# Kernel optimization log

Measured on AMD Instinct MI355X. Metric: run time of the kernel, lower is better.

## Reference

```python
import jax, jax.numpy as jnp
import numpy as np
from jax import lax

H, W = 32, 32
HEADS = 8
EPS_LN = 1e-5


def layer_norm(x, g, b):
    mu = jnp.mean(x, axis=-1, keepdims=True)
    var = jnp.mean((x - mu) ** 2, axis=-1, keepdims=True)
    return (x - mu) * lax.rsqrt(var + EPS_LN) * g + b


def l2norm(x):  # F.normalize along last dim, eps=1e-12
    n = jnp.sqrt(jnp.sum(x * x, axis=-1, keepdims=True))
    return x / jnp.maximum(n, 1e-12)


def channel_attention(x, qkv_w, temp, proj_w, proj_b):
    B, N, C = x.shape
    d = C // HEADS
    qkv = (x @ qkv_w).reshape(B, N, 3, HEADS, d).transpose(2, 0, 3, 1, 4)  # [3,B,h,N,d]
    q, k, v = qkv[0], qkv[1], qkv[2]
    q = l2norm(q.swapaxes(-2, -1))  # [B,h,d,N], normalized over N
    k = l2norm(k.swapaxes(-2, -1))
    v = v.swapaxes(-2, -1)          # [B,h,d,N]
    attn = jnp.einsum('bhdn,bhen->bhde', q, k) * temp  # [B,h,d,d]
    attn = jax.nn.softmax(attn, axis=-1)
    out = jnp.einsum('bhde,bhen->bhdn', attn, v)       # [B,h,d,N]
    out = out.transpose(0, 3, 1, 2).reshape(B, N, C)
    return out @ proj_w + proj_b


def cross_attention(x1, x2, rp_w, rp_b, cn_g, cn_b):
    # head_count = 1 (efficient/linear attention)
    B, N, D = x1.shape
    keys = x2.swapaxes(1, 2)            # [B,D,N]
    values = x1.swapaxes(1, 2)          # [B,D,N]
    key = jax.nn.softmax(keys, axis=2)  # softmax over tokens
    query = jax.nn.softmax(keys, axis=1)  # softmax over channels
    context = jnp.einsum('bdn,ben->bde', key, values)     # [B,Dk,Dv]
    attended = jnp.einsum('bde,bdn->ben', context, query)  # [B,Dv,N]
    agg = attended.reshape(B, D, H, W)
    # 1x1 conv reprojection D -> 2D
    rep = jnp.einsum('bdhw,ed->behw', agg, rp_w) + rp_b[None, :, None, None]
    rep = rep.reshape(B, 2 * D, N).transpose(0, 2, 1)     # [B,N,2D]
    return layer_norm(rep, cn_g, cn_b)


def mix_ffn(x, fc1_w, fc1_b, dw_w, dw_b, fc2_w, fc2_b):
    B, N, _ = x.shape
    c2 = fc1_w.shape[1]
    h1 = x @ fc1_w + fc1_b                                 # [B,N,c2]
    t = h1.swapaxes(1, 2).reshape(B, c2, H, W)
    conv = lax.conv_general_dilated(
        t, dw_w, window_strides=(1, 1), padding='SAME',
        feature_group_count=c2,
        dimension_numbers=('NCHW', 'OIHW', 'NCHW')) + dw_b[None, :, None, None]
    h2 = conv.reshape(B, c2, N).swapaxes(1, 2)             # [B,N,c2]
    return jax.nn.gelu(h2, approximate=False) @ fc2_w + fc2_b


def reference(x1, x2, ln1_g, ln1_b, ca_qkv_w, ca_temp, ca_proj_w, ca_proj_b,
              ln3_g, ln3_b, rp_w, rp_b, cn_g, cn_b, ln2_g, ln2_b,
              fc1_w, fc1_b, dw_w, dw_b, fc2_w, fc2_b):
    # NOTE: original code uses norm1 + channel_attn1 on BOTH streams
    channel1 = x1 + channel_attention(layer_norm(x1, ln1_g, ln1_b), ca_qkv_w, ca_temp, ca_proj_w, ca_proj_b)
    channel2 = x2 + channel_attention(layer_norm(x2, ln1_g, ln1_b), ca_qkv_w, ca_temp, ca_proj_w, ca_proj_b)
    n1 = layer_norm(channel1, ln3_g, ln3_b)
    n2 = layer_norm(channel2, ln3_g, ln3_b)
    attn = cross_attention(n1, n2, rp_w, rp_b, cn_g, cn_b)
    tx = jnp.concatenate([channel1, channel2], axis=2) + attn  # [B,N,2D]
    mx = tx + mix_ffn(layer_norm(tx, ln2_g, ln2_b), fc1_w, fc1_b, dw_w, dw_b, fc2_w, fc2_b)
    return mx


def setup_inputs() -> dict:
    key = jax.random.key(0)
    ks = jax.random.split(key, 8)
    B, N, D = 16, 1024, 384
    s = 0.02
    return {
        'x1': jax.random.normal(ks[0], (B, N, D), jnp.float32),
        'x2': jax.random.normal(ks[1], (B, N, D), jnp.float32),
        'ln1_g': jnp.ones((D,), jnp.float32), 'ln1_b': jnp.zeros((D,), jnp.float32),
        'ca_qkv_w': jax.random.normal(ks[2], (D, 3 * D), jnp.float32) * s,
        'ca_temp': jnp.ones((HEADS, 1, 1), jnp.float32),
        'ca_proj_w': jax.random.normal(ks[3], (D, D), jnp.float32) * s,
        'ca_proj_b': jnp.zeros((D,), jnp.float32),
        'ln3_g': jnp.ones((D,), jnp.float32), 'ln3_b': jnp.zeros((D,), jnp.float32),
        'rp_w': jax.random.normal(ks[4], (2 * D, D), jnp.float32) * s,
        'rp_b': jnp.zeros((2 * D,), jnp.float32),
        'cn_g': jnp.ones((2 * D,), jnp.float32), 'cn_b': jnp.zeros((2 * D,), jnp.float32),
        'ln2_g': jnp.ones((2 * D,), jnp.float32), 'ln2_b': jnp.zeros((2 * D,), jnp.float32),
        'fc1_w': jax.random.normal(ks[5], (2 * D, 4 * D), jnp.float32) * s,
        'fc1_b': jnp.zeros((4 * D,), jnp.float32),
        'dw_w': jax.random.normal(ks[6], (4 * D, 1, 3, 3), jnp.float32) * s,
        'dw_b': jnp.zeros((4 * D,), jnp.float32),
        'fc2_w': jax.random.normal(ks[7], (4 * D, 2 * D), jnp.float32) * s,
        'fc2_b': jnp.zeros((2 * D,), jnp.float32),
    }
```

## Files before the change

### kernel.cpp

```cpp
#include <hip/hip_runtime.h>
#include <math.h>

#define BN 16
#define NN 1024
#define DD 384
#define D2 768
#define C2 1536
#define NHEAD 8
#define DH 48

#define SZ_ND   (BN*NN*DD)
#define SZ_N2D  (BN*NN*D2)
#define SZ_NC2  (BN*NN*C2)

typedef __bf16 bf16x8 __attribute__((ext_vector_type(8)));
typedef float f32x4v __attribute__((ext_vector_type(4)));
typedef unsigned short u16x4 __attribute__((ext_vector_type(4)));

__device__ __forceinline__ unsigned short f2bf(float x){
  unsigned int u = __float_as_uint(x);
  u += 0x7FFFu + ((u >> 16) & 1u);
  return (unsigned short)(u >> 16);
}
__device__ __forceinline__ float bf2f(unsigned short h){
  return __uint_as_float(((unsigned int)h) << 16);
}

__device__ __forceinline__ float blockReduceSum256(float v){
  __shared__ float red[4];
  #pragma unroll
  for (int o=32;o;o>>=1) v += __shfl_down(v,o,64);
  if ((threadIdx.x&63)==0) red[threadIdx.x>>6]=v;
  __syncthreads();
  float r = red[0]+red[1]+red[2]+red[3];
  __syncthreads();
  return r;
}
__device__ __forceinline__ float blockReduceMax256(float v){
  __shared__ float red[4];
  #pragma unroll
  for (int o=32;o;o>>=1) v = fmaxf(v, __shfl_down(v,o,64));
  if ((threadIdx.x&63)==0) red[threadIdx.x>>6]=v;
  __syncthreads();
  float r = fmaxf(fmaxf(red[0],red[1]),fmaxf(red[2],red[3]));
  __syncthreads();
  return r;
// ... 28 lines not shown
  float v=0.f;
  for (int i=threadIdx.x;i<C;i+=256){ float d = x[i]-mu; v += d*d; }
  v = blockReduceSum256(v);
  const float rs = rsqrtf(v/(float)C + 1e-5f);
  unsigned short* ohp = oh + (size_t)row*C;
  unsigned short* olp = ol + (size_t)row*C;
  for (int i=threadIdx.x;i<C;i+=256){
    float val = (x[i]-mu)*rs*g[i] + b[i];
    unsigned short hh = f2bf(val);
    ohp[i] = hh; olp[i] = f2bf(val - bf2f(hh));
  }
}

__global__ __launch_bounds__(256) void rowsoftmax_split_kernel(const float* __restrict__ in,
    unsigned short* __restrict__ oh, unsigned short* __restrict__ ol, int C){
  const int row = blockIdx.x;
  const float* x = in + (size_t)row*C;
  float m = -3.0e38f;
  for (int i=threadIdx.x;i<C;i+=256) m = fmaxf(m, x[i]);
  m = blockReduceMax256(m);
  float s = 0.f;
  for (int i=threadIdx.x;i<C;i+=256) s += expf(x[i]-m);
  s = blockReduceSum256(s);
  const float inv = 1.f/s;
  unsigned short* ohp = oh + (size_t)row*C;
  unsigned short* olp = ol + (size_t)row*C;
  for (int i=threadIdx.x;i<C;i+=256){
    float p = expf(x[i]-m)*inv;
    unsigned short hh = f2bf(p);
    ohp[i] = hh; olp[i] = f2bf(p - bf2f(hh));
  }
}

__global__ __launch_bounds__(256) void colsoftmax_kernel(const float* __restrict__ in,
    float* __restrict__ out){
  const int dl = threadIdx.x & 63;
  const int nc = threadIdx.x >> 6;
  const int d  = blockIdx.x*64 + dl;
  const int b  = blockIdx.y;
  const float* p = in + (size_t)b*NN*DD + d;
  __shared__ float redm[4][64];
  __shared__ float reds[4][64];
  float m = -3.0e38f;
  for (int n=nc*256; n<nc*256+256; n++) m = fmaxf(m, p[(size_t)n*DD]);
  redm[nc][dl] = m; __syncthreads();
  m = fmaxf(fmaxf(redm[0][dl],redm[1][dl]),fmaxf(redm[2][dl],redm[3][dl]));
  float s=0.f;
  for (int n=nc*256;n<nc*256+256;n++) s += expf(p[(size_t)n*DD]-m);
  reds[nc][dl]=s; __syncthreads();
  s = reds[0][dl]+reds[1][dl]+reds[2][dl]+reds[3][dl];
  const float inv = 1.f/s;
  float* q = out + (size_t)b*NN*DD + d;
  for (int n=nc*256;n<nc*256+256;n++) q[(size_t)n*DD] = expf(p[(size_t)n*DD]-m)*inv;
}

__global__ __launch_bounds__(256) void tsplit_kernel(const float* __restrict__ in,
    unsigned short* __restrict__ oh, unsigned short* __restrict__ ol, int R, int Cc){
  const size_t zb = (size_t)blockIdx.z * R * Cc;
  const float* ip = in + zb;
  unsigned short* ohp = oh + zb;
  unsigned short* olp = ol + zb;
  __shared__ float tile[32][33];
  const int c0 = blockIdx.x*32, r0 = blockIdx.y*32;
  const int j = threadIdx.x & 31, i4 = threadIdx.x >> 5;
  #pragma unroll
  for (int s=0;s<4;s++){
    int i = i4*4+s;
    tile[i][j] = ip[(size_t)(r0+i)*Cc + c0 + j];
  }
  __syncthreads();
  #pragma unroll
  for (int s=0;s<4;s++){
    int i = i4*4+s;
    float x = tile[j][i];
    unsigned short h = f2bf(x);
    ohp[(size_t)(c0+i)*R + r0 + j] = h;
    olp[(size_t)(c0+i)*R + r0 + j] = f2bf(x - bf2f(h));
  }
}

__global__ __launch_bounds__(256) void chattn_mfma_kernel(
    const float* __restrict__ qkv, const float* __restrict__ temp,
    unsigned short* __restrict__ coh, unsigned short* __restrict__ col)
{
  const int bh = blockIdx.x, b = bh >> 3, h = bh & 7;
  const int t = threadIdx.x, w = t >> 6, lane = t & 63;
  const int lr = lane & 15, g = lane >> 4;

  __shared__ __align__(16) unsigned char ldsA[27648];
  unsigned short (*Qh)[72] = (unsigned short(*)[72])(ldsA);
  unsigned short (*Ql)[72] = (unsigned short(*)[72])(ldsA + 6912);
  unsigned short (*Kh)[72] = (unsigned short(*)[72])(ldsA + 13824);
  unsigned short (*Kl)[72] = (unsigned short(*)[72])(ldsA + 20736);
  unsigned short (*Vh)[72] = (unsigned short(*)[72])(ldsA);
  unsigned short (*Vl)[72] = (unsigned short(*)[72])(ldsA + 9216);
  __shared__ unsigned short Ph[48][72], Pl[48][72];
  __shared__ float S[48][49];
  __shared__ float qn[48], kn[48];

  const size_t base = (size_t)b*NN*1152 + (size_t)h*48;

  int agrp[3], apr[3], aoff[3];
  #pragma unroll
  for (int l=0;l<3;l++){
    int idx = l*256+t;
    int mo = (idx>=384) ? 1 : 0;
    int a = idx - mo*384;
    agrp[l] = a%12; apr[l] = a/12; aoff[l] = mo*384;
  }

  f32x4v acc[12];
  #pragma unroll
  for (int i=0;i<12;i++) acc[i] = (f32x4v){0.f,0.f,0.f,0.f};

  float4 cur[3][2];
  #pragma unroll
  for (int l=0;l<3;l++){
    const float* p = qkv + base + (size_t)(apr[l]*2)*1152 + aoff[l] + agrp[l]*4;
    cur[l][0] = *(const float4*)p;
    cur[l][1] = *(const float4*)(p+1152);
  }

  for (int nc=0; nc<16; nc++){
    #pragma unroll
    for (int l=0;l<3;l++){
      unsigned short (*Dh)[72] = aoff[l] ? Kh : Qh;
      unsigned short (*Dl)[72] = aoff[l] ? Kl : Ql;
      const float x0[4] = {cur[l][0].x, cur[l][0].y, cur[l][0].z, cur[l][0].w};
      const float x1[4] = {cur[l][1].x, cur[l][1].y, cur[l][1].z, cur[l][1].w};
      #pragma unroll
      for (int c=0;c<4;c++){
        int d = agrp[l]*4+c;
        unsigned short h0 = f2bf(x0[c]), h1 = f2bf(x1[c]);
        unsigned short l0 = f2bf(x0[c]-bf2f(h0)), l1 = f2bf(x1[c]-bf2f(h1));
        *(unsigned int*)&Dh[d][apr[l]*2] = (unsigned)h0 | ((unsigned)h1<<16);
        *(unsigned int*)&Dl[d][apr[l]*2] = (unsigned)l0 | ((unsigned)l1<<16);
      }
    }
    __syncthreads();
    if (nc < 15){
      #pragma unroll
      for (int l=0;l<3;l++){
        const float* p = qkv + base + (size_t)((nc+1)*64 + apr[l]*2)*1152 + aoff[l] + agrp[l]*4;
        cur[l][0] = *(const float4*)p;
        cur[l][1] = *(const float4*)(p+1152);
      }
    }
    if (w < 3){
      #pragma unroll
      for (int ks=0;ks<2;ks++){
        bf16x8 a_h = *(const bf16x8*)&Qh[w*16+lr][ks*32+g*8];
        bf16x8 a_l = *(const bf16x8*)&Ql[w*16+lr][ks*32+g*8];
        #pragma unroll
        for (int c=0;c<3;c++){
          bf16x8 b_h = *(const bf16x8*)&Kh[c*16+lr][ks*32+g*8];
          bf16x8 b_l = *(const bf16x8*)&Kl[c*16+lr][ks*32+g*8];
          acc[c] = __builtin_amdgcn_mfma_f32_16x16x32_bf16(a_h, b_h, acc[c], 0,0,0);
          acc[c] = __builtin_amdgcn_mfma_f32_16x16x32_bf16(a_l, b_h, acc[c], 0,0,0);
          acc[c] = __builtin_amdgcn_mfma_f32_16x16x32_bf16(a_h, b_l, acc[c], 0,0,0);
        }
      }
    } else {
      #pragma unroll
      for (int ks=0;ks<2;ks++){
        #pragma unroll
        for (int c=0;c<3;c++){
          bf16x8 qh_ = *(const bf16x8*)&Qh[c*16+lr][ks*32+g*8];
          bf16x8 ql_ = *(const bf16x8*)&Ql[c*16+lr][ks*32+g*8];
          bf16x8 kh_ = *(const bf16x8*)&Kh[c*16+lr][ks*32+g*8];
          bf16x8 kl_ = *(const bf16x8*)&Kl[c*16+lr][ks*32+g*8];
          acc[c]   = __builtin_amdgcn_mfma_f32_16x16x32_bf16(qh_, qh_, acc[c],   0,0,0);
          acc[3+c] = __builtin_amdgcn_mfma_f32_16x16x32_bf16(qh_, ql_, acc[3+c], 0,0,0);
          acc[6+c] = __builtin_amdgcn_mfma_f32_16x16x32_bf16(kh_, kh_, acc[6+c], 0,0,0);
          acc[9+c] = __builtin_amdgcn_mfma_f32_16x16x32_bf16(kh_, kl_, acc[9+c], 0,0,0);
        }
      }
    }
    __syncthreads();
  }

  const float tp = temp[h];
  if (w == 3){
    if ((lane>>4) == ((lane&15)>>2)){
      int p = lane & 15, r = p & 3;
      #pragma unroll
      for (int c=0;c<3;c++){
        float q2 = fmaxf(acc[c][r]   + 2.f*acc[3+c][r], 0.f);
        float k2 = fmaxf(acc[6+c][r] + 2.f*acc[9+c][r], 0.f);
        qn[c*16+p] = fmaxf(sqrtf(q2), 1e-12f);
        kn[c*16+p] = fmaxf(sqrtf(k2), 1e-12f);
      }
    }
  }
  __syncthreads();
  if (w < 3){
    #pragma unroll
    for (int c=0;c<3;c++){
      #pragma unroll
      for (int r=0;r<4;r++){
        int i = w*16 + g*4 + r, j = c*16 + lr;
        S[i][j] = acc[c][r]*tp/(qn[i]*kn[j]);
      }
    }
  }
  __syncthreads();

  int vgrp[3], vtk[3];
  #pragma unroll
  for (int l=0;l<3;l++){ int idx=l*256+t; vtk[l]=idx/12; vgrp[l]=idx%12; }
  float4 pv[3];
  #pragma unroll
  for (int l=0;l<3;l++)
    pv[l] = *(const float4*)(qkv + base + (size_t)vtk[l]*1152 + 768 + vgrp[l]*4);

  if (t < 48){
    float m = -3.0e38f;
    for (int j=0;j<48;j++) m = fmaxf(m, S[t][j]);
    float s = 0.f;
    for (int j=0;j<48;j++){ float e_ = expf(S[t][j]-m); S[t][j] = e_; s += e_; }
    float inv = 1.f/s;
    for (int j=0;j<48;j++){
      float p = S[t][j]*inv;
      unsigned short hp = f2bf(p);
      Ph[t][j] = hp; Pl[t][j] = f2bf(p - bf2f(hp));
    }
    #pragma unroll
    for (int j=48;j<64;j++){ Ph[t][j]=0; Pl[t][j]=0; }
  } else {
    const u16x4 z4 = (u16x4){0,0,0,0};
    for (int idx=t-48; idx<512; idx+=208){
      int tk = idx>>3, q = idx&7;
      if (q<4) *(u16x4*)&Vh[tk][48+(q&3)*4] = z4;
      else     *(u16x4*)&Vl[tk][48+(q&3)*4] = z4;
    }
  }
  __syncthreads();

  bf16x8 pfh[3][2], pfl[3][2];
  #pragma unroll
  for (int it=0;it<3;it++)
    #pragma unroll
    for (int ks=0;ks<2;ks++){
      pfh[it][ks] = *(const bf16x8*)&Ph[it*16+lr][ks*32+g*8];
      pfl[it][ks] = *(const bf16x8*)&Pl[it*16+lr][ks*32+g*8];
    }

  for (int vc=0; vc<16; vc++){
    #pragma unroll
    for (int l=0;l<3;l++){
      const float xv[4] = {pv[l].x, pv[l].y, pv[l].z, pv[l].w};
      u16x4 hv, lv;
      #pragma unroll
      for (int c=0;c<4;c++){
        unsigned short hh = f2bf(xv[c]);
        hv[c] = hh; lv[c] = f2bf(xv[c] - bf2f(hh));
      }
      *(u16x4*)&Vh[vtk[l]][vgrp[l]*4] = hv;
      *(u16x4*)&Vl[vtk[l]][vgrp[l]*4] = lv;
    }
    __syncthreads();
    if (vc < 15){
      #pragma unroll
      for (int l=0;l<3;l++)
        pv[l] = *(const float4*)(qkv + base + (size_t)((vc+1)*64+vtk[l])*1152 + 768 + vgrp[l]*4);
    }
    bf16x8 vfh[2], vfl[2];
    #pragma unroll
    for (int ks=0;ks<2;ks++){
      vfh[ks] = *(const bf16x8*)&Vh[w*16+lr][ks*32+g*8];
      vfl[ks] = *(const bf16x8*)&Vl[w*16+lr][ks*32+g*8];
    }
    f32x4v o[3];
    #pragma unroll
    for (int it=0;it<3;it++) o[it] = (f32x4v){0.f,0.f,0.f,0.f};
    #pragma unroll
    for (int it=0;it<3;it++)
      #pragma unroll
      for (int ks=0;ks<2;ks++){
        o[it] = __builtin_amdgcn_mfma_f32_16x16x32_bf16(pfh[it][ks], vfh[ks], o[it], 0,0,0);
        o[it] = __builtin_amdgcn_mfma_f32_16x16x32_bf16(pfl[it][ks], vfh[ks], o[it], 0,0,0);
        o[it] = __builtin_amdgcn_mfma_f32_16x16x32_bf16(pfh[it][ks], vfl[ks], o[it], 0,0,0);
      }
    const int n = vc*64 + w*16 + lr;
    #pragma unroll
    for (int it=0;it<3;it++){
      const size_t off = ((size_t)b*NN + n)*DD + h*48 + it*16 + g*4;
      u16x4 hv, lv;
      #pragma unroll
      for (int r=0;r<4;r++){
        float x = o[it][r];
        unsigned short hh = f2bf(x);
        hv[r] = hh; lv[r] = f2bf(x - bf2f(hh));
      }
      *(u16x4*)(coh + off) = hv;
      *(u16x4*)(col + off) = lv;
    }
    __syncthreads();
  }
}

__global__ __launch_bounds__(256) void wconv_t_kernel(const float* __restrict__ in,
    unsigned short* __restrict__ oh, unsigned short* __restrict__ ol, int K, int N){
  __shared__ float tile[32][33];
  const int n0 = blockIdx.x*32, k0 = blockIdx.y*32;
  const int j = threadIdx.x & 31, i4 = threadIdx.x >> 5;
  #pragma unroll
  for (int s=0;s<4;s++){
    int i = i4*4+s;
    tile[i][j] = in[(size_t)(k0+i)*N + n0 + j];
  }
  __syncthreads();
  #pragma unroll
  for (int s=0;s<4;s++){
    int i = i4*4+s;
    float x = tile[j][i];
    unsigned short h = f2bf(x);
    oh[(size_t)(n0+i)*K + k0 + j] = h;
    ol[(size_t)(n0+i)*K + k0 + j] = f2bf(x - bf2f(h));
  }
}

__global__ __launch_bounds__(256) void wconv_kernel(const float* __restrict__ in,
    unsigned short* __restrict__ oh, unsigned short* __restrict__ ol, int n){
  int i = blockIdx.x*256 + threadIdx.x;
  if (i < n){
    float x = in[i];
    unsigned short h = f2bf(x);
    oh[i] = h;
    ol[i] = f2bf(x - bf2f(h));
  }
}

template<bool BIAS_, bool RES_, bool SPLIT_>
__global__ __launch_bounds__(256) void gemm_bf16x3s_kernel(
    const unsigned short* __restrict__ Ah, const unsigned short* __restrict__ Al,
    const unsigned short* __restrict__ Bh, const unsigned short* __restrict__ Bl,
    const float* __restrict__ bias, const float* __restrict__ res,
    float* __restrict__ C, unsigned short* __restrict__ Ch, unsigned short* __restrict__ Cl,
    int M, int N, int K, size_t sAz, size_t sBz, size_t sCz)
{
  const int t = threadIdx.x;
  const int nwg = gridDim.x*gridDim.y;
// ... 99 lines not shown
      for (int mi=0;mi<4;mi++){
        const int r0 = m0 + wm*64 + mi*16 + g*4;
        #pragma unroll
        for (int r=0;r<4;r++){
          float v = acc[mi][ni][r];
          unsigned short hv = f2bf(v);
          const size_t off = (size_t)(r0+r)*N + col;
          Chb[off] = hv;
          Clb[off] = f2bf(v - bf2f(hv));
        }
      }
    }
  } else {
    float* Cb = C + zo*sCz;
    const float* resb = RES_ ? (res + zo*sCz) : nullptr;
    #pragma unroll
    for (int ni=0;ni<4;ni++){
      const int col = n0 + wn*64 + ni*16 + lr;
      const float bb = BIAS_ ? bias[col] : 0.f;
      #pragma unroll
      for (int mi=0;mi<4;mi++){
        const int r0 = m0 + wm*64 + mi*16 + g*4;
        #pragma unroll
        for (int r=0;r<4;r++){
          float v = acc[mi][ni][r] + bb;
          if (RES_) v += resb[(size_t)(r0+r)*N + col];
          Cb[(size_t)(r0+r)*N + col] = v;
        }
      }
    }
  }
}

__global__ __launch_bounds__(256) void ln_concat_kernel(const float* __restrict__ rep,
    const float* __restrict__ g, const float* __restrict__ b,
    const float* __restrict__ ch1, const float* __restrict__ ch2,
    float* __restrict__ tx){
  const int row = blockIdx.x;
  const float* x = rep + (size_t)row*D2;
  float s=0.f;
  for (int i=threadIdx.x;i<D2;i+=256) s += x[i];
  s = blockReduceSum256(s);
  const float mu = s / (float)D2;
  float v=0.f;
  for (int i=threadIdx.x;i<D2;i+=256){ float d = x[i]-mu; v += d*d; }
  v = blockReduceSum256(v);
  const float rs = rsqrtf(v/(float)D2 + 1e-5f);
  float* o = tx + (size_t)row*D2;
  for (int i=threadIdx.x;i<D2;i+=256){
    float val = (x[i]-mu)*rs*g[i] + b[i];
    float rv = (i<DD) ? ch1[(size_t)row*DD + i] : ch2[(size_t)row*DD + i - DD];
    o[i] = val + rv;
  }
}

__global__ __launch_bounds__(256) void dwconv_gelu_kernel(const float* __restrict__ h1,
    const float* __restrict__ w, const float* __restrict__ bias,
    unsigned short* __restrict__ gh, unsigned short* __restrict__ gl){
  const int idx = blockIdx.x*256 + threadIdx.x;
  const int b   = idx / 12288;
  const int r   = idx - b*12288;
  const int hh  = r / 384;
  const int c4  = r - hh*384;
  const int c   = c4*4;
  const float* base = h1 + (size_t)b*NN*C2 + c;
  const size_t obase = ((size_t)b*NN + hh*32)*C2 + c;

  f32x4v wk[9];
  #pragma unroll
  for (int k=0;k<9;k++){
    f32x4v t_;
    #pragma unroll
    for (int q=0;q<4;q++) t_[q] = w[(size_t)(c+q)*9 + k];
    wk[k] = t_;
  }
  f32x4v bvv;
  {
    const float4 bb = *(const float4*)(bias + c);
    bvv = (f32x4v){bb.x, bb.y, bb.z, bb.w};
  }

  const bool hm = (hh > 0), hp = (hh < 31);
  const f32x4v z4 = (f32x4v){0.f,0.f,0.f,0.f};
  const size_t rm = (size_t)((hh-1)*32)*C2;
  const size_t r0 = (size_t)( hh   *32)*C2;
// ... 40 lines not shown

extern "C" void kernel_launch(void* const* d_in, const int* in_sizes, int n_in,
                              void* d_out, int out_size, void* d_ws, size_t ws_size,
                              hipStream_t stream) {
  const float* x1     = (const float*)d_in[0];
  const float* x2     = (const float*)d_in[1];
  const float* ln1_g  = (const float*)d_in[2];
  const float* ln1_b  = (const float*)d_in[3];
  const float* qkv_w  = (const float*)d_in[4];
  const float* ca_temp= (const float*)d_in[5];
  const float* proj_w = (const float*)d_in[6];
  const float* proj_b = (const float*)d_in[7];
  const float* ln3_g  = (const float*)d_in[8];
  const float* ln3_b  = (const float*)d_in[9];
  const float* rp_w   = (const float*)d_in[10];
  const float* rp_b   = (const float*)d_in[11];
  const float* cn_g   = (const float*)d_in[12];
  const float* cn_b   = (const float*)d_in[13];
  const float* ln2_g  = (const float*)d_in[14];
  const float* ln2_b  = (const float*)d_in[15];
  const float* fc1_w  = (const float*)d_in[16];
  const float* fc1_b  = (const float*)d_in[17];
  const float* dw_w   = (const float*)d_in[18];
  const float* dw_b   = (const float*)d_in[19];
  const float* fc2_w  = (const float*)d_in[20];
  const float* fc2_b  = (const float*)d_in[21];
  float* out = (float*)d_out;
  float* W   = (float*)d_ws;

  unsigned short* ycoh = (unsigned short*)W;
  unsigned short* ycol = ycoh + (size_t)SZ_ND;
  unsigned short* coh  = ycoh;
  unsigned short* col  = ycol;
  float* qkvb = W + (size_t)SZ_ND;
  float* ch1  = W + 25165824ull;
  float* ch2  = W + 31457280ull;
  unsigned short* qkvwT_h  = (unsigned short*)(W + 37748736ull);
  unsigned short* qkvwT_l  = qkvwT_h + 442368u;
  unsigned short* projwT_h = qkvwT_l + 442368u;
  unsigned short* projwT_l = projwT_h + 147456u;
  float* n1  = W;
  float* n2  = W + (size_t)SZ_ND;
  float* KS  = W + 2ull*SZ_ND;
  unsigned short* QSh = (unsigned short*)(W + 3ull*SZ_ND);
  unsigned short* QSl = QSh + (size_t)SZ_ND;
  unsigned short* rpw_h = (unsigned short*)(W + 37748736ull);
  unsigned short* rpw_l = rpw_h + 294912u;
  unsigned short* n1t_h = (unsigned short*)(W + 38043648ull);
  unsigned short* n1t_l = n1t_h + (size_t)SZ_ND;
  unsigned short* KSt_h = (unsigned short*)(W + (size_t)SZ_ND);
  unsigned short* KSt_l = KSt_h + (size_t)SZ_ND;
  unsigned short* ctxT_h = (unsigned short*)W;
  unsigned short* ctxT_l = ctxT_h + 2359296u;
  unsigned short* ATbh = (unsigned short*)(W + 2ull*SZ_ND);
  unsigned short* ATbl = ATbh + (size_t)SZ_ND;
  float* rep = W;
  float* txp  = out;
  float* h1   = W;
  unsigned short* y2h = (unsigned short*)(W + 25165824ull);
  unsigned short* y2l = y2h + (size_t)SZ_N2D;
  unsigned short* fc1wT_h = (unsigned short*)(W + 37748736ull);
  unsigned short* fc1wT_l = fc1wT_h + 1179648u;
  unsigned short* gh = (unsigned short*)(W + 25165824ull);
  unsigned short* gl = gh + (size_t)SZ_NC2;
  unsigned short* fc2wT_h = (unsigned short*)W;
  unsigned short* fc2wT_l = fc2wT_h + 1179648u;

  const int M = BN*NN;

  wconv_t_kernel<<<dim3(1152/32, DD/32), dim3(256), 0, stream>>>(qkv_w, qkvwT_h, qkvwT_l, DD, 1152);
  wconv_t_kernel<<<dim3(DD/32, DD/32), dim3(256), 0, stream>>>(proj_w, projwT_h, projwT_l, DD, DD);

  ln_split_kernel<<<dim3(M), dim3(256), 0, stream>>>(x1, ln1_g, ln1_b, ycoh, ycol, DD);
  gemm_bf16x3s_kernel<false,false,false><<<dim3(1152/128, M/128), dim3(256), 0, stream>>>(
      ycoh, ycol, qkvwT_h, qkvwT_l, nullptr, nullptr, qkvb, nullptr, nullptr, M, 1152, DD, 0,0,0);
  chattn_mfma_kernel<<<dim3(BN*NHEAD), dim3(256), 0, stream>>>(qkvb, ca_temp, coh, col);
  gemm_bf16x3s_kernel<true,true,false><<<dim3(DD/128, M/128), dim3(256), 0, stream>>>(
      coh, col, projwT_h, projwT_l, proj_b, x1, ch1, nullptr, nullptr, M, DD, DD, 0,0,0);

  ln_split_kernel<<<dim3(M), dim3(256), 0, stream>>>(x2, ln1_g, ln1_b, ycoh, ycol, DD);
  gemm_bf16x3s_kernel<false,false,false><<<dim3(1152/128, M/128), dim3(256), 0, stream>>>(
      ycoh, ycol, qkvwT_h, qkvwT_l, nullptr, nullptr, qkvb, nullptr, nullptr, M, 1152, DD, 0,0,0);
  chattn_mfma_kernel<<<dim3(BN*NHEAD), dim3(256), 0, stream>>>(qkvb, ca_temp, coh, col);
  gemm_bf16x3s_kernel<true,true,false><<<dim3(DD/128, M/128), dim3(256), 0, stream>>>(
      coh, col, projwT_h, projwT_l, proj_b, x2, ch2, nullptr, nullptr, M, DD, DD, 0,0,0);

  wconv_kernel<<<dim3(294912/256), dim3(256), 0, stream>>>(rp_w, rpw_h, rpw_l, 294912);
  ln_kernel<<<dim3(M), dim3(256), 0, stream>>>(ch1, ln3_g, ln3_b, n1, DD);
  ln_kernel<<<dim3(M), dim3(256), 0, stream>>>(ch2, ln3_g, ln3_b, n2, DD);
  rowsoftmax_split_kernel<<<dim3(M), dim3(256), 0, stream>>>(n2, QSh, QSl, DD);
  colsoftmax_kernel<<<dim3(DD/64, BN), dim3(256), 0, stream>>>(n2, KS);
  tsplit_kernel<<<dim3(DD/32, NN/32, BN), dim3(256), 0, stream>>>(n1, n1t_h, n1t_l, NN, DD);
  tsplit_kernel<<<dim3(DD/32, NN/32, BN), dim3(256), 0, stream>>>(KS, KSt_h, KSt_l, NN, DD);
  gemm_bf16x3s_kernel<false,false,true><<<dim3(DD/128, DD/128, BN), dim3(256), 0, stream>>>(
      n1t_h, n1t_l, KSt_h, KSt_l, nullptr, nullptr, nullptr, ctxT_h, ctxT_l,
      DD, DD, NN, (size_t)DD*NN, (size_t)DD*NN, (size_t)DD*DD);
  gemm_bf16x3s_kernel<false,false,true><<<dim3(DD/128, NN/128, BN), dim3(256), 0, stream>>>(
      QSh, QSl, ctxT_h, ctxT_l, nullptr, nullptr, nullptr, ATbh, ATbl,
      NN, DD, DD, (size_t)NN*DD, (size_t)DD*DD, (size_t)NN*DD);
  gemm_bf16x3s_kernel<true,false,false><<<dim3(D2/128, M/128), dim3(256), 0, stream>>>(
      ATbh, ATbl, rpw_h, rpw_l, rp_b, nullptr, rep, nullptr, nullptr, M, D2, DD, 0,0,0);
  ln_concat_kernel<<<dim3(M), dim3(256), 0, stream>>>(rep, cn_g, cn_b, ch1, ch2, txp);

  wconv_t_kernel<<<dim3(C2/32, D2/32), dim3(256), 0, stream>>>(fc1_w, fc1wT_h, fc1wT_l, D2, C2);
  ln_split_kernel<<<dim3(M), dim3(256), 0, stream>>>(txp, ln2_g, ln2_b, y2h, y2l, D2);
  gemm_bf16x3s_kernel<true,false,false><<<dim3(C2/128, M/128), dim3(256), 0, stream>>>(
      y2h, y2l, fc1wT_h, fc1wT_l, fc1_b, nullptr, h1, nullptr, nullptr, M, C2, D2, 0,0,0);
  dwconv_gelu_kernel<<<dim3(196608/256), dim3(256), 0, stream>>>(h1, dw_w, dw_b, gh, gl);
  wconv_t_kernel<<<dim3(D2/32, C2/32), dim3(256), 0, stream>>>(fc2_w, fc2wT_h, fc2wT_l, C2, D2);
  gemm_bf16x3s_kernel<true,true,false><<<dim3(D2/128, M/128), dim3(256), 0, stream>>>(
      gh, gl, fc2wT_h, fc2wT_l, fc2_b, txp, out, nullptr, nullptr, M, D2, C2, 0,0,0);
}
```

Before: 965.5 us.

## Add 256x256 double-buffered bf16x3 GEMM and fuse LN2 into concat

Adds a 256x256-tile, 512-thread bf16x3 split-precision GEMM with double-buffered XOR-swizzled LDS and workgroup swizzling. It is used for the QKV, reprojection, fc1 and fc2 GEMMs, and the QKV weight is zero-padded to 1280 columns so the grid tiles evenly. Larger tiles aim to raise operand reuse and MFMA density. Separately, the concat LayerNorm now also computes LN2 and writes the split bf16 outputs directly, removing one full pass over the activation. The trade-offs are heavy register and LDS use per block and fewer blocks on the smaller GEMMs (D2=768 gives only 3 column tiles).

```diff
diff --git a/kernel.cpp b/kernel.cpp
--- a/kernel.cpp
+++ b/kernel.cpp
@@ -374,14 +374,14 @@
 }
 
 __global__ __launch_bounds__(256) void wconv_t_kernel(const float* __restrict__ in,
-    unsigned short* __restrict__ oh, unsigned short* __restrict__ ol, int K, int N){
+    unsigned short* __restrict__ oh, unsigned short* __restrict__ ol, int K, int Nin){
   __shared__ float tile[32][33];
   const int n0 = blockIdx.x*32, k0 = blockIdx.y*32;
   const int j = threadIdx.x & 31, i4 = threadIdx.x >> 5;
   #pragma unroll
   for (int s=0;s<4;s++){
     int i = i4*4+s;
-    tile[i][j] = in[(size_t)(k0+i)*N + n0 + j];
+    tile[i][j] = (n0 + j < Nin) ? in[(size_t)(k0+i)*Nin + n0 + j] : 0.f;
   }
   __syncthreads();
   #pragma unroll
@@ -547,25 +547,167 @@
   }
 }
 
-__global__ __launch_bounds__(256) void ln_concat_kernel(const float* __restrict__ rep,
-    const float* __restrict__ g, const float* __restrict__ b,
+template<bool BIAS_, bool RES_>
+__global__ __launch_bounds__(512, 2) void gemm_bf16x3_256_kernel(
+    const unsigned short* __restrict__ Ah, const unsigned short* __restrict__ Al,
+    const unsigned short* __restrict__ Bh, const unsigned short* __restrict__ Bl,
+    const float* __restrict__ bias, const float* __restrict__ res,
+    float* __restrict__ C, int M, int Ncr, int K)
+{
+  const int t = threadIdx.x;
+  const int nwg = gridDim.x*gridDim.y;
+  const int lin = blockIdx.y*gridDim.x + blockIdx.x;
+  const int swz = ((nwg & 7)==0) ? ((lin & 7)*(nwg >> 3) + (lin >> 3)) : lin;
+  const int bx = swz % gridDim.x, by = swz / gridDim.x;
+  const int m0 = by*256, n0 = bx*256;
+
+  __shared__ unsigned short As_h0[256][32], As_l0[256][32];
+  __shared__ unsigned short Bs_h0[256][32], Bs_l0[256][32];
+  __shared__ unsigned short As_h1[256][32], As_l1[256][32];
+  __shared__ unsigned short Bs_h1[256][32], Bs_l1[256][32];
+
+  const unsigned short* Ahb = Ah + (size_t)m0*K;
+  const unsigned short* Alb = Al + (size_t)m0*K;
+  const unsigned short* Bhb = Bh + (size_t)n0*K;
+  const unsigned short* Blb = Bl + (size_t)n0*K;
+
+  f32x4v acc[8][4];
+  #pragma unroll
+  for (int i=0;i<8;i++)
+    #pragma unroll
+    for (int j=0;j<4;j++) acc[i][j] = (f32x4v){0.f,0.f,0.f,0.f};
+
+  const int w  = t >> 6;
+  const int wm = w >> 2, wn = w & 3;
+  const int lr = t & 15, g = (t & 63) >> 4;
+  const int srow = t >> 1;
+  const int kb0  = (t & 1)*2;
+  const int ssw  = (srow >> 1) & 3;
+  const int ks0  = ((kb0+0) ^ ssw)*8;
+  const int ks1  = ((kb0+1) ^ ssw)*8;
+
+  uint4 rAh0,rAh1,rAl0,rAl1,rBh0,rBh1,rBl0,rBl1;
+
+#define LOADT(K0) { \
+    const size_t go0 = (size_t)srow*K + (size_t)(K0) + (size_t)(kb0*8); \
+    rAh0 = *(const uint4*)(Ahb + go0); rAh1 = *(const uint4*)(Ahb + go0 + 8); \
+    rAl0 = *(const uint4*)(Alb + go0); rAl1 = *(const uint4*)(Alb + go0 + 8); \
+    rBh0 = *(const uint4*)(Bhb + go0); rBh1 = *(const uint4*)(Bhb + go0 + 8); \
+    rBl0 = *(const uint4*)(Blb + go0); rBl1 = *(const uint4*)(Blb + go0 + 8); }
+
+#define WRITET(BUF) { \
+    *(uint4*)&As_h##BUF[srow][ks0] = rAh0; *(uint4*)&As_h##BUF[srow][ks1] = rAh1; \
+    *(uint4*)&As_l##BUF[srow][ks0] = rAl0; *(uint4*)&As_l##BUF[srow][ks1] = rAl1; \
+    *(uint4*)&Bs_h##BUF[srow][ks0] = rBh0; *(uint4*)&Bs_h##BUF[srow][ks1] = rBh1; \
+    *(uint4*)&Bs_l##BUF[srow][ks0] = rBl0; *(uint4*)&Bs_l##BUF[srow][ks1] = rBl1; }
+
+#define COMPUTET(BUF) { \
+    bf16x8 bhf[4], blf[4]; \
+    _Pragma("unroll") \
+    for (int ni=0;ni<4;ni++){ \
+      const int rb = wn*64 + ni*16 + lr; \
+      const int kb = (g ^ ((rb>>1)&3))*8; \
+      bhf[ni] = *(const bf16x8*)&Bs_h##BUF[rb][kb]; \
+      blf[ni] = *(const bf16x8*)&Bs_l##BUF[rb][kb]; \
+    } \
+    _Pragma("unroll") \
+    for (int mi=0;mi<8;mi++){ \
+      const int ra = wm*128 + mi*16 + lr; \
+      const int ka = (g ^ ((ra>>1)&3))*8; \
+      bf16x8 ah_ = *(const bf16x8*)&As_h##BUF[ra][ka]; \
+      bf16x8 al_ = *(const bf16x8*)&As_l##BUF[ra][ka]; \
+      _Pragma("unroll") \
+      for (int ni=0;ni<4;ni++){ \
+        f32x4v c_ = acc[mi][ni]; \
+        c_ = __builtin_amdgcn_mfma_f32_16x16x32_bf16(ah_, bhf[ni], c_, 0,0,0); \
+        c_ = __builtin_amdgcn_mfma_f32_16x16x32_bf16(al_, bhf[ni], c_, 0,0,0); \
+        c_ = __builtin_amdgcn_mfma_f32_16x16x32_bf16(ah_, blf[ni], c_, 0,0,0); \
+        acc[mi][ni] = c_; \
+      } \
+    } }
+
+  const int nk = K >> 5;
+  LOADT(0);
+  WRITET(0);
+  LOADT(32);
+  __syncthreads();
+
+  for (int kt = 0; kt < nk; kt += 2){
+    COMPUTET(0);
+    if (kt+1 < nk) WRITET(1);
+    if (kt+2 < nk) LOADT((kt+2)*32);
+    __syncthreads();
+    if (kt+1 < nk) COMPUTET(1);
+    if (kt+2 < nk) WRITET(0);
+    if (kt+3 < nk) LOADT((kt+3)*32);
+    __syncthreads();
+  }
+
+#undef LOADT
+#undef WRITET
+#undef COMPUTET
+
+  #pragma unroll
+  for (int ni=0;ni<4;ni++){
+    const int col = n0 + wn*64 + ni*16 + lr;
+    if (col < Ncr){
+      const float bb = BIAS_ ? bias[col] : 0.f;
+      #pragma unroll
+      for (int mi=0;mi<8;mi++){
+        const int r0 = m0 + wm*128 + mi*16 + g*4;
+        #pragma unroll
+        for (int r=0;r<4;r++){
+          float v = acc[mi][ni][r] + bb;
+          if (RES_) v += res[(size_t)(r0+r)*Ncr + col];
+          C[(size_t)(r0+r)*Ncr + col] = v;
+        }
+      }
+    }
+  }
+}
+
+__global__ __launch_bounds__(256) void ln_concat_ln2_kernel(const float* __restrict__ rep,
+    const float* __restrict__ g1, const float* __restrict__ b1,
     const float* __restrict__ ch1, const float* __restrict__ ch2,
-    float* __restrict__ tx){
+    const float* __restrict__ g2, const float* __restrict__ b2,
+    float* __restrict__ tx, unsigned short* __restrict__ y2h, unsigned short* __restrict__ y2l){
   const int row = blockIdx.x;
   const float* x = rep + (size_t)row*D2;
+  float xv[3];
   float s=0.f;
-  for (int i=threadIdx.x;i<D2;i+=256) s += x[i];
+  #pragma unroll
+  for (int q=0;q<3;q++){ xv[q] = x[threadIdx.x + q*256]; s += xv[q]; }
   s = blockReduceSum256(s);
   const float mu = s / (float)D2;
   float v=0.f;
-  for (int i=threadIdx.x;i<D2;i+=256){ float d = x[i]-mu; v += d*d; }
+  #pragma unroll
+  for (int q=0;q<3;q++){ float d = xv[q]-mu; v += d*d; }
   v = blockReduceSum256(v);
   const float rs = rsqrtf(v/(float)D2 + 1e-5f);
-  float* o = tx + (size_t)row*D2;
-  for (int i=threadIdx.x;i<D2;i+=256){
-    float val = (x[i]-mu)*rs*g[i] + b[i];
+  float tv[3];
+  #pragma unroll
+  for (int q=0;q<3;q++){
+    int i = threadIdx.x + q*256;
+    float val = (xv[q]-mu)*rs*g1[i] + b1[i];
     float rv = (i<DD) ? ch1[(size_t)row*DD + i] : ch2[(size_t)row*DD + i - DD];
-    o[i] = val + rv;
+    tv[q] = val + rv;
+    tx[(size_t)row*D2 + i] = tv[q];
+  }
+  float s2 = tv[0]+tv[1]+tv[2];
+  s2 = blockReduceSum256(s2);
+  const float mu2 = s2 / (float)D2;
+  float v2=0.f;
+  #pragma unroll
+  for (int q=0;q<3;q++){ float d = tv[q]-mu2; v2 += d*d; }
+  v2 = blockReduceSum256(v2);
+  const float rs2 = rsqrtf(v2/(float)D2 + 1e-5f);
+  #pragma unroll
+  for (int q=0;q<3;q++){
+    int i = threadIdx.x + q*256;
+    float y = (tv[q]-mu2)*rs2*g2[i] + b2[i];
+    unsigned short hh = f2bf(y);
+    y2h[(size_t)row*D2 + i] = hh;
+    y2l[(size_t)row*D2 + i] = f2bf(y - bf2f(hh));
   }
 }
 
@@ -676,8 +818,8 @@
   float* ch1  = W + 25165824ull;
   float* ch2  = W + 31457280ull;
   unsigned short* qkvwT_h  = (unsigned short*)(W + 37748736ull);
-  unsigned short* qkvwT_l  = qkvwT_h + 442368u;
-  unsigned short* projwT_h = qkvwT_l + 442368u;
+  unsigned short* qkvwT_l  = qkvwT_h + 491520u;
+  unsigned short* projwT_h = qkvwT_l + 491520u;
   unsigned short* projwT_l = projwT_h + 147456u;
   float* n1  = W;
   float* n2  = W + (size_t)SZ_ND;
@@ -708,19 +850,19 @@
 
   const int M = BN*NN;
 
-  wconv_t_kernel<<<dim3(1152/32, DD/32), dim3(256), 0, stream>>>(qkv_w, qkvwT_h, qkvwT_l, DD, 1152);
+  wconv_t_kernel<<<dim3(1280/32, DD/32), dim3(256), 0, stream>>>(qkv_w, qkvwT_h, qkvwT_l, DD, 1152);
   wconv_t_kernel<<<dim3(DD/32, DD/32), dim3(256), 0, stream>>>(proj_w, projwT_h, projwT_l, DD, DD);
 
   ln_split_kernel<<<dim3(M), dim3(256), 0, stream>>>(x1, ln1_g, ln1_b, ycoh, ycol, DD);
-  gemm_bf16x3s_kernel<false,false,false><<<dim3(1152/128, M/128), dim3(256), 0, stream>>>(
-      ycoh, ycol, qkvwT_h, qkvwT_l, nullptr, nullptr, qkvb, nullptr, nullptr, M, 1152, DD, 0,0,0);
+  gemm_bf16x3_256_kernel<false,false><<<dim3(1280/256, M/256), dim3(512), 0, stream>>>(
+      ycoh, ycol, qkvwT_h, qkvwT_l, nullptr, nullptr, qkvb, M, 1152, DD);
   chattn_mfma_kernel<<<dim3(BN*NHEAD), dim3(256), 0, stream>>>(qkvb, ca_temp, coh, col);
   gemm_bf16x3s_kernel<true,true,false><<<dim3(DD/128, M/128), dim3(256), 0, stream>>>(
       coh, col, projwT_h, projwT_l, proj_b, x1, ch1, nullptr, nullptr, M, DD, DD, 0,0,0);
 
   ln_split_kernel<<<dim3(M), dim3(256), 0, stream>>>(x2, ln1_g, ln1_b, ycoh, ycol, DD);
-  gemm_bf16x3s_kernel<false,false,false><<<dim3(1152/128, M/128), dim3(256), 0, stream>>>(
-      ycoh, ycol, qkvwT_h, qkvwT_l, nullptr, nullptr, qkvb, nullptr, nullptr, M, 1152, DD, 0,0,0);
+  gemm_bf16x3_256_kernel<false,false><<<dim3(1280/256, M/256), dim3(512), 0, stream>>>(
+      ycoh, ycol, qkvwT_h, qkvwT_l, nullptr, nullptr, qkvb, M, 1152, DD);
   chattn_mfma_kernel<<<dim3(BN*NHEAD), dim3(256), 0, stream>>>(qkvb, ca_temp, coh, col);
   gemm_bf16x3s_kernel<true,true,false><<<dim3(DD/128, M/128), dim3(256), 0, stream>>>(
       coh, col, projwT_h, projwT_l, proj_b, x2, ch2, nullptr, nullptr, M, DD, DD, 0,0,0);
@@ -738,16 +880,16 @@
   gemm_bf16x3s_kernel<false,false,true><<<dim3(DD/128, NN/128, BN), dim3(256), 0, stream>>>(
       QSh, QSl, ctxT_h, ctxT_l, nullptr, nullptr, nullptr, ATbh, ATbl,
       NN, DD, DD, (size_t)NN*DD, (size_t)DD*DD, (size_t)NN*DD);
-  gemm_bf16x3s_kernel<true,false,false><<<dim3(D2/128, M/128), dim3(256), 0, stream>>>(
-      ATbh, ATbl, rpw_h, rpw_l, rp_b, nullptr, rep, nullptr, nullptr, M, D2, DD, 0,0,0);
-  ln_concat_kernel<<<dim3(M), dim3(256), 0, stream>>>(rep, cn_g, cn_b, ch1, ch2, txp);
+  gemm_bf16x3_256_kernel<true,false><<<dim3(D2/256, M/256), dim3(512), 0, stream>>>(
+      ATbh, ATbl, rpw_h, rpw_l, rp_b, nullptr, rep, M, D2, DD);
+  ln_concat_ln2_kernel<<<dim3(M), dim3(256), 0, stream>>>(
+      rep, cn_g, cn_b, ch1, ch2, ln2_g, ln2_b, txp, y2h, y2l);
 
   wconv_t_kernel<<<dim3(C2/32, D2/32), dim3(256), 0, stream>>>(fc1_w, fc1wT_h, fc1wT_l, D2, C2);
-  ln_split_kernel<<<dim3(M), dim3(256), 0, stream>>>(txp, ln2_g, ln2_b, y2h, y2l, D2);
-  gemm_bf16x3s_kernel<true,false,false><<<dim3(C2/128, M/128), dim3(256), 0, stream>>>(
-      y2h, y2l, fc1wT_h, fc1wT_l, fc1_b, nullptr, h1, nullptr, nullptr, M, C2, D2, 0,0,0);
+  gemm_bf16x3_256_kernel<true,false><<<dim3(C2/256, M/256), dim3(512), 0, stream>>>(
+      y2h, y2l, fc1wT_h, fc1wT_l, fc1_b, nullptr, h1, M, C2, D2);
   dwconv_gelu_kernel<<<dim3(196608/256), dim3(256), 0, stream>>>(h1, dw_w, dw_b, gh, gl);
   wconv_t_kernel<<<dim3(D2/32, C2/32), dim3(256), 0, stream>>>(fc2_w, fc2wT_h, fc2wT_l, C2, D2);
-  gemm_bf16x3s_kernel<true,true,false><<<dim3(D2/128, M/128), dim3(256), 0, stream>>>(
-      gh, gl, fc2wT_h, fc2wT_l, fc2_b, txp, out, nullptr, nullptr, M, D2, C2, 0,0,0);
-}
+  gemm_bf16x3_256_kernel<true,true><<<dim3(D2/256, M/256), dim3(512), 0, stream>>>(
+      gh, gl, fc2wT_h, fc2wT_l, fc2_b, txp, out, M, D2, C2);
+}
```

After: 1.056 ms. 1.09x slower.

## Fuse split/transposes into producers: bf16 QKV output, colsoftmax-transpose, LN-concat-LN2

Applied to the files above, without the earlier changes.

The QKV GEMM now writes hi/lo bf16 split outputs directly, so the channel-attention kernel loads bf16 pairs instead of fp32 and skips its own split. Column softmax writes transposed hi/lo bf16 directly, which removes a separate tsplit pass. The concat layer norm is fused with the following LN2 split, which drops one kernel and its reread of txp. The aim is to cut memory traffic and launches, but the colsoftmax transposed store is strided per thread and may coalesce poorly. The workspace layout also changes, so buffers must not overlap.

```diff
diff --git a/kernel.cpp b/kernel.cpp
--- a/kernel.cpp
+++ b/kernel.cpp
@@ -12,6 +12,7 @@
 #define SZ_ND   (BN*NN*DD)
 #define SZ_N2D  (BN*NN*D2)
 #define SZ_NC2  (BN*NN*C2)
+#define SZ_QKV  (BN*NN*3*DD)
 
 typedef __bf16 bf16x8 __attribute__((ext_vector_type(8)));
 typedef float f32x4v __attribute__((ext_vector_type(4)));
@@ -106,8 +107,8 @@
   }
 }
 
-__global__ __launch_bounds__(256) void colsoftmax_kernel(const float* __restrict__ in,
-    float* __restrict__ out){
+__global__ __launch_bounds__(256) void colsoftmax_tsplit_kernel(const float* __restrict__ in,
+    unsigned short* __restrict__ oh, unsigned short* __restrict__ ol){
   const int dl = threadIdx.x & 63;
   const int nc = threadIdx.x >> 6;
   const int d  = blockIdx.x*64 + dl;
@@ -124,8 +125,13 @@
   reds[nc][dl]=s; __syncthreads();
   s = reds[0][dl]+reds[1][dl]+reds[2][dl]+reds[3][dl];
   const float inv = 1.f/s;
-  float* q = out + (size_t)b*NN*DD + d;
-  for (int n=nc*256;n<nc*256+256;n++) q[(size_t)n*DD] = expf(p[(size_t)n*DD]-m)*inv;
+  unsigned short* qh = oh + ((size_t)b*DD + d)*NN;
+  unsigned short* ql = ol + ((size_t)b*DD + d)*NN;
+  for (int n=nc*256;n<nc*256+256;n++){
+    float val = expf(p[(size_t)n*DD]-m)*inv;
+    unsigned short hh = f2bf(val);
+    qh[n] = hh; ql[n] = f2bf(val - bf2f(hh));
+  }
 }
 
 __global__ __launch_bounds__(256) void tsplit_kernel(const float* __restrict__ in,
@@ -154,7 +160,8 @@
 }
 
 __global__ __launch_bounds__(256) void chattn_mfma_kernel(
-    const float* __restrict__ qkv, const float* __restrict__ temp,
+    const unsigned short* __restrict__ qh, const unsigned short* __restrict__ ql,
+    const float* __restrict__ temp,
     unsigned short* __restrict__ coh, unsigned short* __restrict__ col)
 {
   const int bh = blockIdx.x, b = bh >> 3, h = bh & 7;
@@ -187,12 +194,14 @@
   #pragma unroll
   for (int i=0;i<12;i++) acc[i] = (f32x4v){0.f,0.f,0.f,0.f};
 
-  float4 cur[3][2];
+  u16x4 ch0[3], ch1_[3], cl0[3], cl1[3];
   #pragma unroll
   for (int l=0;l<3;l++){
-    const float* p = qkv + base + (size_t)(apr[l]*2)*1152 + aoff[l] + agrp[l]*4;
-    cur[l][0] = *(const float4*)p;
-    cur[l][1] = *(const float4*)(p+1152);
+    const size_t a = base + (size_t)(apr[l]*2)*1152 + aoff[l] + agrp[l]*4;
+    ch0[l] = *(const u16x4*)(qh + a);
+    ch1_[l]= *(const u16x4*)(qh + a + 1152);
+    cl0[l] = *(const u16x4*)(ql + a);
+    cl1[l] = *(const u16x4*)(ql + a + 1152);
   }
 
   for (int nc=0; nc<16; nc++){
@@ -200,24 +209,22 @@
     for (int l=0;l<3;l++){
       unsigned short (*Dh)[72] = aoff[l] ? Kh : Qh;
       unsigned short (*Dl)[72] = aoff[l] ? Kl : Ql;
-      const float x0[4] = {cur[l][0].x, cur[l][0].y, cur[l][0].z, cur[l][0].w};
-      const float x1[4] = {cur[l][1].x, cur[l][1].y, cur[l][1].z, cur[l][1].w};
       #pragma unroll
       for (int c=0;c<4;c++){
         int d = agrp[l]*4+c;
-        unsigned short h0 = f2bf(x0[c]), h1 = f2bf(x1[c]);
-        unsigned short l0 = f2bf(x0[c]-bf2f(h0)), l1 = f2bf(x1[c]-bf2f(h1));
-        *(unsigned int*)&Dh[d][apr[l]*2] = (unsigned)h0 | ((unsigned)h1<<16);
-        *(unsigned int*)&Dl[d][apr[l]*2] = (unsigned)l0 | ((unsigned)l1<<16);
+        *(unsigned int*)&Dh[d][apr[l]*2] = (unsigned)ch0[l][c] | ((unsigned)ch1_[l][c]<<16);
+        *(unsigned int*)&Dl[d][apr[l]*2] = (unsigned)cl0[l][c] | ((unsigned)cl1[l][c]<<16);
       }
     }
     __syncthreads();
     if (nc < 15){
       #pragma unroll
       for (int l=0;l<3;l++){
-        const float* p = qkv + base + (size_t)((nc+1)*64 + apr[l]*2)*1152 + aoff[l] + agrp[l]*4;
-        cur[l][0] = *(const float4*)p;
-        cur[l][1] = *(const float4*)(p+1152);
+        const size_t a = base + (size_t)((nc+1)*64 + apr[l]*2)*1152 + aoff[l] + agrp[l]*4;
+        ch0[l] = *(const u16x4*)(qh + a);
+        ch1_[l]= *(const u16x4*)(qh + a + 1152);
+        cl0[l] = *(const u16x4*)(ql + a);
+        cl1[l] = *(const u16x4*)(ql + a + 1152);
       }
     }
     if (w < 3){
@@ -282,10 +289,13 @@
   int vgrp[3], vtk[3];
   #pragma unroll
   for (int l=0;l<3;l++){ int idx=l*256+t; vtk[l]=idx/12; vgrp[l]=idx%12; }
-  float4 pv[3];
-  #pragma unroll
-  for (int l=0;l<3;l++)
-    pv[l] = *(const float4*)(qkv + base + (size_t)vtk[l]*1152 + 768 + vgrp[l]*4);
+  u16x4 pvh[3], pvl[3];
+  #pragma unroll
+  for (int l=0;l<3;l++){
+    const size_t a = base + (size_t)vtk[l]*1152 + 768 + vgrp[l]*4;
+    pvh[l] = *(const u16x4*)(qh + a);
+    pvl[l] = *(const u16x4*)(ql + a);
+  }
 
   if (t < 48){
     float m = -3.0e38f;
@@ -322,21 +332,17 @@
   for (int vc=0; vc<16; vc++){
     #pragma unroll
     for (int l=0;l<3;l++){
-      const float xv[4] = {pv[l].x, pv[l].y, pv[l].z, pv[l].w};
-      u16x4 hv, lv;
-      #pragma unroll
-      for (int c=0;c<4;c++){
-        unsigned short hh = f2bf(xv[c]);
-        hv[c] = hh; lv[c] = f2bf(xv[c] - bf2f(hh));
-      }
-      *(u16x4*)&Vh[vtk[l]][vgrp[l]*4] = hv;
-      *(u16x4*)&Vl[vtk[l]][vgrp[l]*4] = lv;
+      *(u16x4*)&Vh[vtk[l]][vgrp[l]*4] = pvh[l];
+      *(u16x4*)&Vl[vtk[l]][vgrp[l]*4] = pvl[l];
     }
     __syncthreads();
     if (vc < 15){
       #pragma unroll
-      for (int l=0;l<3;l++)
-        pv[l] = *(const float4*)(qkv + base + (size_t)((vc+1)*64+vtk[l])*1152 + 768 + vgrp[l]*4);
+      for (int l=0;l<3;l++){
+        const size_t a = base + (size_t)((vc+1)*64+vtk[l])*1152 + 768 + vgrp[l]*4;
+        pvh[l] = *(const u16x4*)(qh + a);
+        pvl[l] = *(const u16x4*)(ql + a);
+      }
     }
     bf16x8 vfh[2], vfl[2];
     #pragma unroll
@@ -374,14 +380,14 @@
 }
 
 __global__ __launch_bounds__(256) void wconv_t_kernel(const float* __restrict__ in,
-    unsigned short* __restrict__ oh, unsigned short* __restrict__ ol, int K, int N){
+    unsigned short* __restrict__ oh, unsigned short* __restrict__ ol, int K, int Nin){
   __shared__ float tile[32][33];
   const int n0 = blockIdx.x*32, k0 = blockIdx.y*32;
   const int j = threadIdx.x & 31, i4 = threadIdx.x >> 5;
   #pragma unroll
   for (int s=0;s<4;s++){
     int i = i4*4+s;
-    tile[i][j] = in[(size_t)(k0+i)*N + n0 + j];
+    tile[i][j] = (n0 + j < Nin) ? in[(size_t)(k0+i)*Nin + n0 + j] : 0.f;
   }
   __syncthreads();
   #pragma unroll
@@ -547,25 +553,48 @@
   }
 }
 
-__global__ __launch_bounds__(256) void ln_concat_kernel(const float* __restrict__ rep,
-    const float* __restrict__ g, const float* __restrict__ b,
+__global__ __launch_bounds__(256) void ln_concat_ln2_kernel(const float* __restrict__ rep,
+    const float* __restrict__ g1, const float* __restrict__ b1,
     const float* __restrict__ ch1, const float* __restrict__ ch2,
-    float* __restrict__ tx){
+    const float* __restrict__ g2, const float* __restrict__ b2,
+    float* __restrict__ tx, unsigned short* __restrict__ y2h, unsigned short* __restrict__ y2l){
   const int row = blockIdx.x;
   const float* x = rep + (size_t)row*D2;
+  float xv[3];
   float s=0.f;
-  for (int i=threadIdx.x;i<D2;i+=256) s += x[i];
+  #pragma unroll
+  for (int q=0;q<3;q++){ xv[q] = x[threadIdx.x + q*256]; s += xv[q]; }
   s = blockReduceSum256(s);
   const float mu = s / (float)D2;
   float v=0.f;
-  for (int i=threadIdx.x;i<D2;i+=256){ float d = x[i]-mu; v += d*d; }
+  #pragma unroll
+  for (int q=0;q<3;q++){ float d = xv[q]-mu; v += d*d; }
   v = blockReduceSum256(v);
   const float rs = rsqrtf(v/(float)D2 + 1e-5f);
-  float* o = tx + (size_t)row*D2;
-  for (int i=threadIdx.x;i<D2;i+=256){
-    float val = (x[i]-mu)*rs*g[i] + b[i];
+  float tv[3];
+  #pragma unroll
+  for (int q=0;q<3;q++){
+    int i = threadIdx.x + q*256;
+    float val = (xv[q]-mu)*rs*g1[i] + b1[i];
     float rv = (i<DD) ? ch1[(size_t)row*DD + i] : ch2[(size_t)row*DD + i - DD];
-    o[i] = val + rv;
+    tv[q] = val + rv;
+    tx[(size_t)row*D2 + i] = tv[q];
+  }
+  float s2 = tv[0]+tv[1]+tv[2];
+  s2 = blockReduceSum256(s2);
+  const float mu2 = s2 / (float)D2;
+  float v2=0.f;
+  #pragma unroll
+  for (int q=0;q<3;q++){ float d = tv[q]-mu2; v2 += d*d; }
+  v2 = blockReduceSum256(v2);
+  const float rs2 = rsqrtf(v2/(float)D2 + 1e-5f);
+  #pragma unroll
+  for (int q=0;q<3;q++){
+    int i = threadIdx.x + q*256;
+    float y = (tv[q]-mu2)*rs2*g2[i] + b2[i];
+    unsigned short hh = f2bf(y);
+    y2h[(size_t)row*D2 + i] = hh;
+    y2l[(size_t)row*D2 + i] = f2bf(y - bf2f(hh));
   }
 }
 
@@ -672,7 +701,8 @@
   unsigned short* ycol = ycoh + (size_t)SZ_ND;
   unsigned short* coh  = ycoh;
   unsigned short* col  = ycol;
-  float* qkvb = W + (size_t)SZ_ND;
+  unsigned short* qkvh = (unsigned short*)(W + (size_t)SZ_ND);
+  unsigned short* qkvl = qkvh + (size_t)SZ_QKV;
   float* ch1  = W + 25165824ull;
   float* ch2  = W + 31457280ull;
   unsigned short* qkvwT_h  = (unsigned short*)(W + 37748736ull);
@@ -681,15 +711,14 @@
   unsigned short* projwT_l = projwT_h + 147456u;
   float* n1  = W;
   float* n2  = W + (size_t)SZ_ND;
-  float* KS  = W + 2ull*SZ_ND;
+  unsigned short* KSt_h = (unsigned short*)(W + 2ull*SZ_ND);
+  unsigned short* KSt_l = KSt_h + (size_t)SZ_ND;
   unsigned short* QSh = (unsigned short*)(W + 3ull*SZ_ND);
   unsigned short* QSl = QSh + (size_t)SZ_ND;
   unsigned short* rpw_h = (unsigned short*)(W + 37748736ull);
   unsigned short* rpw_l = rpw_h + 294912u;
   unsigned short* n1t_h = (unsigned short*)(W + 38043648ull);
   unsigned short* n1t_l = n1t_h + (size_t)SZ_ND;
-  unsigned short* KSt_h = (unsigned short*)(W + (size_t)SZ_ND);
-  unsigned short* KSt_l = KSt_h + (size_t)SZ_ND;
   unsigned short* ctxT_h = (unsigned short*)W;
   unsigned short* ctxT_l = ctxT_h + 2359296u;
   unsigned short* ATbh = (unsigned short*)(W + 2ull*SZ_ND);
@@ -712,16 +741,16 @@
   wconv_t_kernel<<<dim3(DD/32, DD/32), dim3(256), 0, stream>>>(proj_w, projwT_h, projwT_l, DD, DD);
 
   ln_split_kernel<<<dim3(M), dim3(256), 0, stream>>>(x1, ln1_g, ln1_b, ycoh, ycol, DD);
-  gemm_bf16x3s_kernel<false,false,false><<<dim3(1152/128, M/128), dim3(256), 0, stream>>>(
-      ycoh, ycol, qkvwT_h, qkvwT_l, nullptr, nullptr, qkvb, nullptr, nullptr, M, 1152, DD, 0,0,0);
-  chattn_mfma_kernel<<<dim3(BN*NHEAD), dim3(256), 0, stream>>>(qkvb, ca_temp, coh, col);
+  gemm_bf16x3s_kernel<false,false,true><<<dim3(1152/128, M/128), dim3(256), 0, stream>>>(
+      ycoh, ycol, qkvwT_h, qkvwT_l, nullptr, nullptr, nullptr, qkvh, qkvl, M, 1152, DD, 0,0,0);
+  chattn_mfma_kernel<<<dim3(BN*NHEAD), dim3(256), 0, stream>>>(qkvh, qkvl, ca_temp, coh, col);
   gemm_bf16x3s_kernel<true,true,false><<<dim3(DD/128, M/128), dim3(256), 0, stream>>>(
       coh, col, projwT_h, projwT_l, proj_b, x1, ch1, nullptr, nullptr, M, DD, DD, 0,0,0);
 
   ln_split_kernel<<<dim3(M), dim3(256), 0, stream>>>(x2, ln1_g, ln1_b, ycoh, ycol, DD);
-  gemm_bf16x3s_kernel<false,false,false><<<dim3(1152/128, M/128), dim3(256), 0, stream>>>(
-      ycoh, ycol, qkvwT_h, qkvwT_l, nullptr, nullptr, qkvb, nullptr, nullptr, M, 1152, DD, 0,0,0);
-  chattn_mfma_kernel<<<dim3(BN*NHEAD), dim3(256), 0, stream>>>(qkvb, ca_temp, coh, col);
+  gemm_bf16x3s_kernel<false,false,true><<<dim3(1152/128, M/128), dim3(256), 0, stream>>>(
+      ycoh, ycol, qkvwT_h, qkvwT_l, nullptr, nullptr, nullptr, qkvh, qkvl, M, 1152, DD, 0,0,0);
+  chattn_mfma_kernel<<<dim3(BN*NHEAD), dim3(256), 0, stream>>>(qkvh, qkvl, ca_temp, coh, col);
   gemm_bf16x3s_kernel<true,true,false><<<dim3(DD/128, M/128), dim3(256), 0, stream>>>(
       coh, col, projwT_h, projwT_l, proj_b, x2, ch2, nullptr, nullptr, M, DD, DD, 0,0,0);
 
@@ -729,9 +758,8 @@
   ln_kernel<<<dim3(M), dim3(256), 0, stream>>>(ch1, ln3_g, ln3_b, n1, DD);
   ln_kernel<<<dim3(M), dim3(256), 0, stream>>>(ch2, ln3_g, ln3_b, n2, DD);
   rowsoftmax_split_kernel<<<dim3(M), dim3(256), 0, stream>>>(n2, QSh, QSl, DD);
-  colsoftmax_kernel<<<dim3(DD/64, BN), dim3(256), 0, stream>>>(n2, KS);
+  colsoftmax_tsplit_kernel<<<dim3(DD/64, BN), dim3(256), 0, stream>>>(n2, KSt_h, KSt_l);
   tsplit_kernel<<<dim3(DD/32, NN/32, BN), dim3(256), 0, stream>>>(n1, n1t_h, n1t_l, NN, DD);
-  tsplit_kernel<<<dim3(DD/32, NN/32, BN), dim3(256), 0, stream>>>(KS, KSt_h, KSt_l, NN, DD);
   gemm_bf16x3s_kernel<false,false,true><<<dim3(DD/128, DD/128, BN), dim3(256), 0, stream>>>(
       n1t_h, n1t_l, KSt_h, KSt_l, nullptr, nullptr, nullptr, ctxT_h, ctxT_l,
       DD, DD, NN, (size_t)DD*NN, (size_t)DD*NN, (size_t)DD*DD);
@@ -740,10 +768,10 @@
       NN, DD, DD, (size_t)NN*DD, (size_t)DD*DD, (size_t)NN*DD);
   gemm_bf16x3s_kernel<true,false,false><<<dim3(D2/128, M/128), dim3(256), 0, stream>>>(
       ATbh, ATbl, rpw_h, rpw_l, rp_b, nullptr, rep, nullptr, nullptr, M, D2, DD, 0,0,0);
-  ln_concat_kernel<<<dim3(M), dim3(256), 0, stream>>>(rep, cn_g, cn_b, ch1, ch2, txp);
+  ln_concat_ln2_kernel<<<dim3(M), dim3(256), 0, stream>>>(
+      rep, cn_g, cn_b, ch1, ch2, ln2_g, ln2_b, txp, y2h, y2l);
 
   wconv_t_kernel<<<dim3(C2/32, D2/32), dim3(256), 0, stream>>>(fc1_w, fc1wT_h, fc1wT_l, D2, C2);
-  ln_split_kernel<<<dim3(M), dim3(256), 0, stream>>>(txp, ln2_g, ln2_b, y2h, y2l, D2);
   gemm_bf16x3s_kernel<true,false,false><<<dim3(C2/128, M/128), dim3(256), 0, stream>>>(
       y2h, y2l, fc1wT_h, fc1wT_l, fc1_b, nullptr, h1, nullptr, nullptr, M, C2, D2, 0,0,0);
   dwconv_gelu_kernel<<<dim3(196608/256), dim3(256), 0, stream>>>(h1, dw_w, dw_b, gh, gl);
```

After: 975.9 us. No clear change (+1.1%).
